# Kernel optimization log

Hardware: AMD Instinct MI355X
Metric: run time of the kernel (lower is better)

Reference implementation:

```python
import jax, jax.numpy as jnp
import numpy as np

WSCALE = 0.02  # keep conv outputs / softmax logits in a sane range

def _conv3x3(x, w):
    # x: [B,C,H,W], w: [O,I,3,3], stride 1, padding 1 (SAME), no bias
    return jax.lax.conv_general_dilated(
        x, w, window_strides=(1, 1), padding='SAME',
        dimension_numbers=('NCHW', 'OIHW', 'NCHW'))

def setup_inputs() -> dict:
    key = jax.random.key(0)
    ks = jax.random.split(key, 5)
    B, C, V, T = 8, 256, 256, 64
    Cq, C1 = C // 8, C // 2
    x = jax.random.normal(ks[0], (B, C, V, T), dtype=jnp.float32)
    wq = jax.random.normal(ks[1], (Cq, C, 3, 3), dtype=jnp.float32) * WSCALE
    wk = jax.random.normal(ks[2], (Cq, C, 3, 3), dtype=jnp.float32) * WSCALE
    wv = jax.random.normal(ks[3], (C1, C, 3, 3), dtype=jnp.float32) * WSCALE
    wo = jax.random.normal(ks[4], (C, C1, 3, 3), dtype=jnp.float32) * WSCALE
    sigma = jnp.ones((1,), dtype=jnp.float32)
    return {'x': x, 'wq': wq, 'wk': wk, 'wv': wv, 'wo': wo, 'sigma': sigma}

def reference(x, wq, wk, wv, wo, sigma):
    # x: [B, C, V, T]; attention over V, independent per (B, T) slice
    q = _conv3x3(x, wq)   # [B, Cq, V, T]
    k = _conv3x3(x, wk)   # [B, Cq, V, T]
    v = _conv3x3(x, wv)   # [B, C1, V, T]
    # permute(0,3,2,1): [B, T, V, C]
    q = jnp.transpose(q, (0, 3, 2, 1))
    k = jnp.transpose(k, (0, 3, 2, 1))
    v = jnp.transpose(v, (0, 3, 2, 1))
    # scores: [B, T, V, V]; softmax over last dim (original softmax dim=2 of [B*T,V,V])
    attn = jax.nn.softmax(jnp.einsum('btvc,btuc->btvu', q, k), axis=-1)
    av = jnp.einsum('btvu,btuc->btvc', attn, v)        # [B, T, V, C1]
    av = jnp.transpose(av, (0, 3, 2, 1))               # [B, C1, V, T]
    out = _conv3x3(av, wo)                             # [B, C, V, T]
    return x + sigma * out
```

## Files before the change

kernel.cpp:

```cpp
#include <hip/hip_runtime.h>
#include <hip/hip_bf16.h>
#include <cstdint>

#define B_  8
#define C_  256
#define V_  256
#define T_  64
#define CQ_ 32
#define C1_ 128

typedef float  floatx4 __attribute__((ext_vector_type(4)));
typedef __bf16 bf16x8  __attribute__((ext_vector_type(8)));

static __device__ __forceinline__ ushort f2bf(float f) {
    union { float f; uint32_t u; } cv; cv.f = f;
    const uint32_t u = cv.u;
    return (ushort)((u + 0x7FFFu + ((u >> 16) & 1u)) >> 16);
}
static __device__ __forceinline__ void bf2x(uint32_t p, float& f0, float& f1) {
    union { uint32_t u; float f; } a, b;
    a.u = p << 16; b.u = p & 0xffff0000u;
    f0 = a.f; f1 = b.f;
}

__global__ __launch_bounds__(256) void transpose_x(
    const float* __restrict__ x, ushort* __restrict__ xT)
{
    __shared__ float xs[256 * 65];
    const int tid = threadIdx.x;
    const int v = blockIdx.x & 255;
    const int b = blockIdx.x >> 8;

    for (int i = tid; i < 16384; i += 256) {
        const int t = i & 63, c = i >> 6;
        xs[c * 65 + t] = x[(((size_t)b * C_ + c) * V_ + v) * T_ + t];
    }
    __syncthreads();
    for (int i = tid; i < 16384; i += 256) {
        const int c = i & 255, t = i >> 8;
        xT[(((size_t)b * V_ + v) * T_ + t) * C_ + c] = f2bf(xs[c * 65 + t]);
    }
}

__global__ __launch_bounds__(256) void pack_weights(
    const float* __restrict__ wq, const float* __restrict__ wk,
    const float* __restrict__ wv, const float* __restrict__ wo,
    ushort* __restrict__ Wqkv, ushort* __restrict__ Wo)
{
    const int r = blockIdx.x;
    const int tid = threadIdx.x;
    const float* src; ushort* dst; int Klen;
    if (r < 192) {
        if (r < 32)      src = wq + (size_t)r * 2304;
        else if (r < 64) src = wk + (size_t)(r - 32) * 2304;
        else             src = wv + (size_t)(r - 64) * 2304;
        dst = Wqkv + (size_t)r * 2304; Klen = 2304;
    } else {
        src = wo + (size_t)(r - 192) * 1152;
        dst = Wo + (size_t)(r - 192) * 1152; Klen = 1152;
    }
    for (int k = tid; k < Klen; k += 256) {
        const int cc = k / 288, rem = k % 288;
        const int tap = rem >> 5, ci = rem & 31;
        const int c = cc * 32 + ci;
        dst[k] = f2bf(src[c * 9 + tap]);
    }
}

__global__ __launch_bounds__(256) void conv_qkv_mfma(
    const ushort* __restrict__ xT, const ushort* __restrict__ Wqkv,
    ushort* __restrict__ qb, ushort* __restrict__ kb, ushort* __restrict__ vb)
{
    __shared__ __align__(16) ushort Bs[4 * 66 * 40];
    __shared__ __align__(16) ushort As[64 * 296];

    const int tid  = threadIdx.x;
    const int lane = tid & 63;
    const int wave = tid >> 6;
    const int wave_m = (wave >> 1) * 32;
    const int wave_n = (wave & 1) * 64;
    const int nl = lane & 15;
    const int q8 = lane >> 4;

    int idx = blockIdx.x;
    const int og = idx % 3; idx /= 3;
    const int v2 = idx & 127;
    const int b  = idx >> 7;
    const int v0 = v2 * 2;

    floatx4 acc[2][4];
    #pragma unroll
    for (int i = 0; i < 2; i++)
        #pragma unroll
        for (int j = 0; j < 4; j++) acc[i][j] = (floatx4)0.f;

    const int rr = tid >> 6, ts = tid & 63;
    const int vsrc = v0 - 1 + rr;
    const int ar = tid >> 2, sub = tid & 3;

    for (int cc = 0; cc < 8; cc++) {
        const int c0 = cc * 32;
        __syncthreads();
        {
            ushort* bdst = &Bs[(rr * 66 + 1 + ts) * 40];
            if (vsrc >= 0 && vsrc < V_) {
                const ushort* src = &xT[(((size_t)b * V_ + vsrc) * T_ + ts) * C_ + c0];
                *(uint4*)(bdst + 0)  = *(const uint4*)(src + 0);
                *(uint4*)(bdst + 8)  = *(const uint4*)(src + 8);
                *(uint4*)(bdst + 16) = *(const uint4*)(src + 16);
                *(uint4*)(bdst + 24) = *(const uint4*)(src + 24);
            } else {
                const uint4 z = {0u, 0u, 0u, 0u};
                *(uint4*)(bdst + 0) = z; *(uint4*)(bdst + 8) = z;
                *(uint4*)(bdst + 16) = z; *(uint4*)(bdst + 24) = z;
            }
            if (tid < 8) {
                const int r2 = tid >> 1, side = (tid & 1) * 65;
                ushort* zp = &Bs[(r2 * 66 + side) * 40];
                const uint4 z = {0u, 0u, 0u, 0u};
                *(uint4*)(zp + 0) = z; *(uint4*)(zp + 8) = z;
                *(uint4*)(zp + 16) = z; *(uint4*)(zp + 24) = z;
            }
        }
        {
            const ushort* asrc = &Wqkv[(size_t)(og * 64 + ar) * 2304 + cc * 288];
            ushort* adst = &As[ar * 296];
            #pragma unroll
            for (int j = 0; j < 9; j++) {
                const int w8 = (sub + j * 4) * 8;
                *(uint4*)(adst + w8) = *(const uint4*)(asrc + w8);
            }
        }
        __syncthreads();

        #pragma unroll
        for (int tap = 0; tap < 9; tap++) {
            const int dv = tap / 3, dt = tap % 3;
            const bf16x8 a0 = *(const bf16x8*)&As[(wave_m + nl) * 296 + tap * 32 + q8 * 8];
            const bf16x8 a1 = *(const bf16x8*)&As[(wave_m + 16 + nl) * 296 + tap * 32 + q8 * 8];
            #pragma unroll
            for (int nt = 0; nt < 4; nt++) {
                const int n0 = wave_n + nt * 16;
                const int vv = n0 >> 6, tt0 = n0 & 63;
                const bf16x8 bf = *(const bf16x8*)
                    &Bs[((vv + dv) * 66 + tt0 + nl + dt) * 40 + q8 * 8];
                acc[0][nt] = __builtin_amdgcn_mfma_f32_16x16x32_bf16(a0, bf, acc[0][nt], 0, 0, 0);
                acc[1][nt] = __builtin_amdgcn_mfma_f32_16x16x32_bf16(a1, bf, acc[1][nt], 0, 0, 0);
            }
        }
    }

    #pragma unroll
    for (int mt = 0; mt < 2; mt++) {
        const int g0 = og * 64 + wave_m + mt * 16 + q8 * 4;
        ushort* buf; int cbase, Cb;
        if (g0 < 32)      { buf = qb; cbase = g0;      Cb = CQ_; }
        else if (g0 < 64) { buf = kb; cbase = g0 - 32; Cb = CQ_; }
        else              { buf = vb; cbase = g0 - 64; Cb = C1_; }
        #pragma unroll
        for (int nt = 0; nt < 4; nt++) {
            const int n = wave_n + nt * 16 + nl;
            const int vv = n >> 6, tt = n & 63;
            const floatx4 A = acc[mt][nt];
            ushort4 o;
            o.x = f2bf(A[0]); o.y = f2bf(A[1]); o.z = f2bf(A[2]); o.w = f2bf(A[3]);
            *(ushort4*)&buf[(((size_t)b * V_ + v0 + vv) * T_ + tt) * Cb + cbase] = o;
        }
    }
}

__global__ __launch_bounds__(256) void conv_o_mfma(
    const ushort* __restrict__ avT, const ushort* __restrict__ Wo,
    const float* __restrict__ x, const float* __restrict__ sigma,
    float* __restrict__ out)
{
    __shared__ __align__(16) ushort Bs[4 * 66 * 40];
    __shared__ __align__(16) ushort As[64 * 296];

    const int tid  = threadIdx.x;
    const int lane = tid & 63;
    const int wave = tid >> 6;
    const int wave_m = (wave >> 1) * 32;
    const int wave_n = (wave & 1) * 64;
    const int nl = lane & 15;
    const int q8 = lane >> 4;

    int idx = blockIdx.x;
    const int og = idx & 3; idx >>= 2;
    const int v2 = idx & 127;
    const int b  = idx >> 7;
    const int v0 = v2 * 2;

    floatx4 acc[2][4];
    #pragma unroll
    for (int i = 0; i < 2; i++)
        #pragma unroll
        for (int j = 0; j < 4; j++) acc[i][j] = (floatx4)0.f;

    const int rr = tid >> 6, ts = tid & 63;
    const int vsrc = v0 - 1 + rr;
    const int ar = tid >> 2, sub = tid & 3;

    for (int cc = 0; cc < 4; cc++) {
        const int c0 = cc * 32;
        __syncthreads();
        {
            ushort* bdst = &Bs[(rr * 66 + 1 + ts) * 40];
            if (vsrc >= 0 && vsrc < V_) {
                const ushort* src = &avT[(((size_t)b * V_ + vsrc) * T_ + ts) * C1_ + c0];
                *(uint4*)(bdst + 0)  = *(const uint4*)(src + 0);
                *(uint4*)(bdst + 8)  = *(const uint4*)(src + 8);
                *(uint4*)(bdst + 16) = *(const uint4*)(src + 16);
                *(uint4*)(bdst + 24) = *(const uint4*)(src + 24);
            } else {
                const uint4 z = {0u, 0u, 0u, 0u};
                *(uint4*)(bdst + 0) = z; *(uint4*)(bdst + 8) = z;
                *(uint4*)(bdst + 16) = z; *(uint4*)(bdst + 24) = z;
            }
            if (tid < 8) {
                const int r2 = tid >> 1, side = (tid & 1) * 65;
                ushort* zp = &Bs[(r2 * 66 + side) * 40];
                const uint4 z = {0u, 0u, 0u, 0u};
                *(uint4*)(zp + 0) = z; *(uint4*)(zp + 8) = z;
                *(uint4*)(zp + 16) = z; *(uint4*)(zp + 24) = z;
            }
        }
        {
            const ushort* asrc = &Wo[(size_t)(og * 64 + ar) * 1152 + cc * 288];
            ushort* adst = &As[ar * 296];
            #pragma unroll
            for (int j = 0; j < 9; j++) {
                const int w8 = (sub + j * 4) * 8;
                *(uint4*)(adst + w8) = *(const uint4*)(asrc + w8);
            }
        }
        __syncthreads();

        #pragma unroll
        for (int tap = 0; tap < 9; tap++) {
            const int dv = tap / 3, dt = tap % 3;
            const bf16x8 a0 = *(const bf16x8*)&As[(wave_m + nl) * 296 + tap * 32 + q8 * 8];
            const bf16x8 a1 = *(const bf16x8*)&As[(wave_m + 16 + nl) * 296 + tap * 32 + q8 * 8];
            #pragma unroll
            for (int nt = 0; nt < 4; nt++) {
                const int n0 = wave_n + nt * 16;
                const int vv = n0 >> 6, tt0 = n0 & 63;
                const bf16x8 bf = *(const bf16x8*)
                    &Bs[((vv + dv) * 66 + tt0 + nl + dt) * 40 + q8 * 8];
                acc[0][nt] = __builtin_amdgcn_mfma_f32_16x16x32_bf16(a0, bf, acc[0][nt], 0, 0, 0);
                acc[1][nt] = __builtin_amdgcn_mfma_f32_16x16x32_bf16(a1, bf, acc[1][nt], 0, 0, 0);
            }
        }
    }

    const float sg = sigma[0];
    #pragma unroll
    for (int mt = 0; mt < 2; mt++) {
        const int cb = og * 64 + wave_m + mt * 16 + q8 * 4;
        #pragma unroll
        for (int nt = 0; nt < 4; nt++) {
            const int n = wave_n + nt * 16 + nl;
            const int vv = n >> 6, tt = n & 63;
            const floatx4 A = acc[mt][nt];
            #pragma unroll
            for (int r = 0; r < 4; r++) {
                const size_t o = (((size_t)b * C_ + cb + r) * V_ + (v0 + vv)) * T_ + tt;
                out[o] = x[o] + sg * A[r];
            }
        }
    }
}

#define L2E 1.44269504f

__global__ __launch_bounds__(256, 1) void attn_mfma(
    const ushort* __restrict__ qb, const ushort* __restrict__ kb,
    const ushort* __restrict__ vb, ushort* __restrict__ avT)
{
    __shared__ __align__(16) ushort Ksh[256 * 40];
    __shared__ __align__(16) ushort Vt[128 * 264];
    __shared__ __align__(16) ushort Psh[4][64 * 72];

    const int tid  = threadIdx.x;
    const int lane = tid & 63;
    const int w    = tid >> 6;
    const int l15  = lane & 15;
    const int q8   = lane >> 4;
    const int bt = blockIdx.x;
    const int b = bt >> 6, t = bt & 63;

    {
        const ushort* kp = &kb[(((size_t)b * 256 + tid) * 64 + t) * 32];
        #pragma unroll
        for (int j = 0; j < 4; j++)
            *(uint4*)&Ksh[tid * 40 + j * 8] = *(const uint4*)(kp + j * 8);
    }
    {
        const int c8 = tid & 15;
        #pragma unroll
        for (int it = 0; it < 8; it++) {
            const int up = it * 16 + (tid >> 4);
            const ushort* vp0 = &vb[(((size_t)b * 256 + up * 2) * 64 + t) * 128 + c8 * 8];
            uint4 ra = *(const uint4*)vp0;
            uint4 rb = *(const uint4*)(vp0 + 64 * 128);
            const ushort* pa = (const ushort*)&ra;
            const ushort* pb = (const ushort*)&rb;
            const int g = up >> 2, sub = up & 3;
            #pragma unroll
            for (int j = 0; j < 8; j++) {
                const int c = c8 * 8 + j;
                const uint word = (uint)pa[j] | ((uint)pb[j] << 16);
                *(uint*)((char*)(Vt + c * 264) + ((g ^ (c8 & 7)) * 16 + sub * 4)) = word;
            }
        }
    }
    bf16x8 qf[4];
    #pragma unroll
    for (int vt = 0; vt < 4; vt++) {
        const int v = w * 64 + vt * 16 + l15;
        qf[vt] = *(const bf16x8*)&qb[(((size_t)b * 256 + v) * 64 + t) * 32 + q8 * 8];
    }
    __syncthreads();

    floatx4 accO[8][4];
    #pragma unroll
    for (int ct = 0; ct < 8; ct++)
        #pragma unroll
        for (int vt = 0; vt < 4; vt++) accO[ct][vt] = (floatx4)0.f;
    float m2[4] = {-3e38f, -3e38f, -3e38f, -3e38f};
    float lr[4] = {0.f, 0.f, 0.f, 0.f};
    ushort* Pw = Psh[w];

    for (int ch = 0; ch < 4; ch++) {
        const int u0 = ch * 64;
        floatx4 s[4][4];
        #pragma unroll
        for (int ut = 0; ut < 4; ut++) {
            const bf16x8 kf = *(const bf16x8*)&Ksh[(u0 + ut * 16 + l15) * 40 + q8 * 8];
            #pragma unroll
            for (int vt = 0; vt < 4; vt++) {
                floatx4 z = (floatx4)0.f;
                s[ut][vt] = __builtin_amdgcn_mfma_f32_16x16x32_bf16(kf, qf[vt], z, 0, 0, 0);
            }
        }
        #pragma unroll
        for (int vt = 0; vt < 4; vt++) {
            #pragma unroll
            for (int ut = 0; ut < 4; ut++)
                #pragma unroll
                for (int r = 0; r < 4; r++) s[ut][vt][r] *= L2E;
            float cm = -3e38f;
            #pragma unroll
            for (int ut = 0; ut < 4; ut++)
                #pragma unroll
                for (int r = 0; r < 4; r++) cm = fmaxf(cm, s[ut][vt][r]);
            cm = fmaxf(cm, __shfl_xor(cm, 16));
            cm = fmaxf(cm, __shfl_xor(cm, 32));
            const float mn = fmaxf(m2[vt], cm);
            const float alpha = __builtin_amdgcn_exp2f(m2[vt] - mn);
            float csum = 0.f;
            #pragma unroll
            for (int ut = 0; ut < 4; ut++)
                #pragma unroll
                for (int r = 0; r < 4; r++) {
                    const float p = __builtin_amdgcn_exp2f(s[ut][vt][r] - mn);
                    s[ut][vt][r] = p;
                    csum += p;
                }
            csum += __shfl_xor(csum, 16);
            csum += __shfl_xor(csum, 32);
            lr[vt] = lr[vt] * alpha + csum;
            m2[vt] = mn;
            #pragma unroll
            for (int ct = 0; ct < 8; ct++)
                #pragma unroll
                for (int r = 0; r < 4; r++) accO[ct][vt][r] *= alpha;
            const int vrow = vt * 16 + l15;
            #pragma unroll
            for (int ut = 0; ut < 4; ut++) {
                const uint w01 = (uint)f2bf(s[ut][vt][0]) | ((uint)f2bf(s[ut][vt][1]) << 16);
                const uint w23 = (uint)f2bf(s[ut][vt][2]) | ((uint)f2bf(s[ut][vt][3]) << 16);
                ushort* pp = Pw + vrow * 72 + ut * 16 + q8 * 4;
                *(uint*)pp = w01;
                *(uint*)(pp + 2) = w23;
            }
        }
        #pragma unroll
        for (int kc = 0; kc < 2; kc++) {
            bf16x8 pf[4];
            #pragma unroll
            for (int vt = 0; vt < 4; vt++)
                pf[vt] = *(const bf16x8*)&Pw[(vt * 16 + l15) * 72 + kc * 32 + q8 * 8];
            #pragma unroll
            for (int ct = 0; ct < 8; ct++) {
                const int c = ct * 16 + l15;
                const int ublk = (u0 + kc * 32) / 8 + q8;
                const bf16x8 vf = *(const bf16x8*)
                    ((const char*)(Vt + c * 264) + ((ublk ^ ((c >> 3) & 7)) * 16));
                #pragma unroll
                for (int vt = 0; vt < 4; vt++)
                    accO[ct][vt] = __builtin_amdgcn_mfma_f32_16x16x32_bf16(vf, pf[vt], accO[ct][vt], 0, 0, 0);
            }
        }
    }

    float inv[4];
    #pragma unroll
    for (int vt = 0; vt < 4; vt++) inv[vt] = 1.f / lr[vt];

    #pragma unroll
    for (int half = 0; half < 2; half++) {
        #pragma unroll
        for (int ct4 = 0; ct4 < 4; ct4++) {
            const int ct = half * 4 + ct4;
            #pragma unroll
            for (int vt = 0; vt < 4; vt++) {
                ushort4 o;
                o.x = f2bf(accO[ct][vt][0] * inv[vt]);
                o.y = f2bf(accO[ct][vt][1] * inv[vt]);
                o.z = f2bf(accO[ct][vt][2] * inv[vt]);
                o.w = f2bf(accO[ct][vt][3] * inv[vt]);
                *(ushort4*)&Pw[(vt * 16 + l15) * 72 + ct4 * 16 + q8 * 4] = o;
            }
        }
        const size_t dst = (((size_t)b * 256 + w * 64 + lane) * 64 + t) * 128 + half * 64;
        #pragma unroll
        for (int j = 0; j < 8; j++)
            *(uint4*)&avT[dst + j * 8] = *(const uint4*)&Pw[lane * 72 + j * 8];
    }
}

extern "C" void kernel_launch(void* const* d_in, const int* in_sizes, int n_in,
                              void* d_out, int out_size, void* d_ws, size_t ws_size,
                              hipStream_t stream)
{
    const float* x     = (const float*)d_in[0];
    const float* wq    = (const float*)d_in[1];
    const float* wk    = (const float*)d_in[2];
    const float* wv    = (const float*)d_in[3];
    const float* wo    = (const float*)d_in[4];
    const float* sigma = (const float*)d_in[5];
    float* out = (float*)d_out;

    ushort* ws   = (ushort*)d_ws;
    ushort* xT   = ws;  ws += (size_t)B_ * V_ * T_ * C_;
    ushort* qb   = ws;  ws += (size_t)B_ * V_ * T_ * CQ_;
    ushort* kb   = ws;  ws += (size_t)B_ * V_ * T_ * CQ_;
    ushort* vb   = ws;  ws += (size_t)B_ * V_ * T_ * C1_;
    ushort* avT  = ws;  ws += (size_t)B_ * V_ * T_ * C1_;
    ushort* Wqkv = ws;  ws += 192 * 2304;
    ushort* Wo   = ws;  ws += 256 * 1152;

    transpose_x <<<B_ * V_, 256, 0, stream>>>(x, xT);
    pack_weights<<<448, 256, 0, stream>>>(wq, wk, wv, wo, Wqkv, Wo);
    conv_qkv_mfma<<<B_ * 128 * 3, 256, 0, stream>>>(xT, Wqkv, qb, kb, vb);
    attn_mfma   <<<B_ * T_, 256, 0, stream>>>(qb, kb, vb, avT);
    conv_o_mfma <<<B_ * 128 * 4, 256, 0, stream>>>(avT, Wo, x, sigma, out);
}
```

Before: 580.3 us.

## Prepack weights in MFMA fragment order and restructure conv tiles with register prefetch

Weights are repacked into per-lane MFMA A-fragment order so the conv kernels read A operands straight from global/L2 instead of staging them in shared memory. Each block now covers 4 V rows (one per wave) and all 64 output channels, using a 6-row halo in LDS. The next channel chunk's activations are prefetched into registers while the current chunk computes. This removes the LDS traffic and barriers for weights and cuts halo redundancy, at the cost of more accumulator registers and more global weight reads per wave.

New measurement: 504.6 us. 1.15x faster.

```diff
diff --git a/kernel.cpp b/kernel.cpp
--- a/kernel.cpp
+++ b/kernel.cpp
@@ -17,11 +17,6 @@
     const uint32_t u = cv.u;
     return (ushort)((u + 0x7FFFu + ((u >> 16) & 1u)) >> 16);
 }
-static __device__ __forceinline__ void bf2x(uint32_t p, float& f0, float& f1) {
-    union { uint32_t u; float f; } a, b;
-    a.u = p << 16; b.u = p & 0xffff0000u;
-    f0 = a.f; f1 = b.f;
-}
 
 __global__ __launch_bounds__(256) void transpose_x(
     const float* __restrict__ x, ushort* __restrict__ xT)
@@ -47,23 +42,36 @@
     const float* __restrict__ wv, const float* __restrict__ wo,
     ushort* __restrict__ Wqkv, ushort* __restrict__ Wo)
 {
-    const int r = blockIdx.x;
-    const int tid = threadIdx.x;
-    const float* src; ushort* dst; int Klen;
-    if (r < 192) {
-        if (r < 32)      src = wq + (size_t)r * 2304;
-        else if (r < 64) src = wk + (size_t)(r - 32) * 2304;
-        else             src = wv + (size_t)(r - 64) * 2304;
-        dst = Wqkv + (size_t)r * 2304; Klen = 2304;
-    } else {
-        src = wo + (size_t)(r - 192) * 1152;
-        dst = Wo + (size_t)(r - 192) * 1152; Klen = 1152;
-    }
-    for (int k = tid; k < Klen; k += 256) {
-        const int cc = k / 288, rem = k % 288;
-        const int tap = rem >> 5, ci = rem & 31;
-        const int c = cc * 32 + ci;
-        dst[k] = f2bf(src[c * 9 + tap]);
+    const int tid = blockIdx.x * 256 + threadIdx.x;
+    const int total1 = 442368, total2 = 294912;
+    for (int idx = tid; idx < total1 + total2; idx += gridDim.x * 256) {
+        if (idx < total1) {
+            int i = idx;
+            const int e = i & 7;      i >>= 3;
+            const int lane = i & 63;  i >>= 6;
+            const int mtile = i & 3;  i >>= 2;
+            const int tap = i % 9;    i /= 9;
+            const int cc = i & 7;
+            const int og = i >> 3;
+            const int r = og * 64 + mtile * 16 + (lane & 15);
+            const int c = cc * 32 + (lane >> 4) * 8 + e;
+            const float* srow;
+            if (r < 32)      srow = wq + (size_t)r * 2304;
+            else if (r < 64) srow = wk + (size_t)(r - 32) * 2304;
+            else             srow = wv + (size_t)(r - 64) * 2304;
+            Wqkv[idx] = f2bf(srow[c * 9 + tap]);
+        } else {
+            int i = idx - total1;
+            const int e = i & 7;      i >>= 3;
+            const int lane = i & 63;  i >>= 6;
+            const int mtile = i & 3;  i >>= 2;
+            const int tap = i % 9;    i /= 9;
+            const int cc = i & 3;
+            const int og = i >> 2;
+            const int r = og * 64 + mtile * 16 + (lane & 15);
+            const int c = cc * 32 + (lane >> 4) * 8 + e;
+            Wo[idx - total1] = f2bf(wo[(size_t)r * 1152 + c * 9 + tap]);
+        }
     }
 }
 
@@ -71,100 +79,103 @@
     const ushort* __restrict__ xT, const ushort* __restrict__ Wqkv,
     ushort* __restrict__ qb, ushort* __restrict__ kb, ushort* __restrict__ vb)
 {
-    __shared__ __align__(16) ushort Bs[4 * 66 * 40];
-    __shared__ __align__(16) ushort As[64 * 296];
+    __shared__ __align__(16) ushort Bs[6 * 66 * 40];
 
     const int tid  = threadIdx.x;
     const int lane = tid & 63;
-    const int wave = tid >> 6;
-    const int wave_m = (wave >> 1) * 32;
-    const int wave_n = (wave & 1) * 64;
-    const int nl = lane & 15;
-    const int q8 = lane >> 4;
-
-    int idx = blockIdx.x;
-    const int og = idx % 3; idx /= 3;
-    const int v2 = idx & 127;
-    const int b  = idx >> 7;
-    const int v0 = v2 * 2;
-
-    floatx4 acc[2][4];
-    #pragma unroll
-    for (int i = 0; i < 2; i++)
+    const int w    = tid >> 6;
+    const int nl   = lane & 15;
+    const int q8   = lane >> 4;
+
+    const int og  = blockIdx.x >> 9;
+    const int rem = blockIdx.x & 511;
+    const int vg  = rem >> 3;
+    const int b   = rem & 7;
+    const int v0  = vg * 4;
+
+    floatx4 acc[4][4];
+    #pragma unroll
+    for (int i = 0; i < 4; i++)
         #pragma unroll
         for (int j = 0; j < 4; j++) acc[i][j] = (floatx4)0.f;
 
-    const int rr = tid >> 6, ts = tid & 63;
-    const int vsrc = v0 - 1 + rr;
-    const int ar = tid >> 2, sub = tid & 3;
+    const int t4 = tid >> 2, c4 = tid & 3;
+    ushort* const bdst = &Bs[(1 + t4) * 40 + c4 * 8];
+    const ushort* const xb  = &xT[(((size_t)b * V_) * T_ + t4) * C_ + c4 * 8];
+    const ushort* const Wog = Wqkv + (size_t)og * 147456 + lane * 8;
+
+    if (tid < 12) {
+        const int r = tid >> 1, side = (tid & 1) * 65;
+        ushort* zp = &Bs[(r * 66 + side) * 40];
+        const uint4 z = {0u, 0u, 0u, 0u};
+        *(uint4*)(zp + 0) = z; *(uint4*)(zp + 8) = z;
+        *(uint4*)(zp + 16) = z; *(uint4*)(zp + 24) = z;
+    }
+
+    const uint4 z4 = {0u, 0u, 0u, 0u};
+    uint4 s0, s1, s2, s3, s4, s5;
+
+#define QPF(CC) do {                                                          \
+    const int co_ = (CC) * 32;                                                \
+    s0 = (v0 >= 1)  ? *(const uint4*)(xb + (size_t)(v0 - 1) * (T_ * C_) + co_) : z4; \
+    s1 =              *(const uint4*)(xb + (size_t)(v0    ) * (T_ * C_) + co_);      \
+    s2 =              *(const uint4*)(xb + (size_t)(v0 + 1) * (T_ * C_) + co_);      \
+    s3 =              *(const uint4*)(xb + (size_t)(v0 + 2) * (T_ * C_) + co_);      \
+    s4 =              *(const uint4*)(xb + (size_t)(v0 + 3) * (T_ * C_) + co_);      \
+    s5 = (v0 < 252) ? *(const uint4*)(xb + (size_t)(v0 + 4) * (T_ * C_) + co_) : z4; \
+} while (0)
+
+    QPF(0);
 
     for (int cc = 0; cc < 8; cc++) {
-        const int c0 = cc * 32;
         __syncthreads();
-        {
-            ushort* bdst = &Bs[(rr * 66 + 1 + ts) * 40];
-            if (vsrc >= 0 && vsrc < V_) {
-                const ushort* src = &xT[(((size_t)b * V_ + vsrc) * T_ + ts) * C_ + c0];
-                *(uint4*)(bdst + 0)  = *(const uint4*)(src + 0);
-                *(uint4*)(bdst + 8)  = *(const uint4*)(src + 8);
-                *(uint4*)(bdst + 16) = *(const uint4*)(src + 16);
-                *(uint4*)(bdst + 24) = *(const uint4*)(src + 24);
-            } else {
-                const uint4 z = {0u, 0u, 0u, 0u};
-                *(uint4*)(bdst + 0) = z; *(uint4*)(bdst + 8) = z;
-                *(uint4*)(bdst + 16) = z; *(uint4*)(bdst + 24) = z;
-            }
-            if (tid < 8) {
-                const int r2 = tid >> 1, side = (tid & 1) * 65;
-                ushort* zp = &Bs[(r2 * 66 + side) * 40];
-                const uint4 z = {0u, 0u, 0u, 0u};
-                *(uint4*)(zp + 0) = z; *(uint4*)(zp + 8) = z;
-                *(uint4*)(zp + 16) = z; *(uint4*)(zp + 24) = z;
-            }
-        }
-        {
-            const ushort* asrc = &Wqkv[(size_t)(og * 64 + ar) * 2304 + cc * 288];
-            ushort* adst = &As[ar * 296];
-            #pragma unroll
-            for (int j = 0; j < 9; j++) {
-                const int w8 = (sub + j * 4) * 8;
-                *(uint4*)(adst + w8) = *(const uint4*)(asrc + w8);
-            }
-        }
+        *(uint4*)(bdst + 0 * 2640) = s0;
+        *(uint4*)(bdst + 1 * 2640) = s1;
+        *(uint4*)(bdst + 2 * 2640) = s2;
+        *(uint4*)(bdst + 3 * 2640) = s3;
+        *(uint4*)(bdst + 4 * 2640) = s4;
+        *(uint4*)(bdst + 5 * 2640) = s5;
         __syncthreads();
-
+        if (cc < 7) QPF(cc + 1);
+
+        const ushort* const Wcc = Wog + cc * 18432;
         #pragma unroll
         for (int tap = 0; tap < 9; tap++) {
             const int dv = tap / 3, dt = tap % 3;
-            const bf16x8 a0 = *(const bf16x8*)&As[(wave_m + nl) * 296 + tap * 32 + q8 * 8];
-            const bf16x8 a1 = *(const bf16x8*)&As[(wave_m + 16 + nl) * 296 + tap * 32 + q8 * 8];
+            bf16x8 bfr[4];
+            #pragma unroll
+            for (int nt = 0; nt < 4; nt++)
+                bfr[nt] = *(const bf16x8*)
+                    &Bs[((w + dv) * 66 + nt * 16 + nl + dt) * 40 + q8 * 8];
+            const bf16x8 a0 = *(const bf16x8*)(Wcc + tap * 2048 + 0 * 512);
+            const bf16x8 a1 = *(const bf16x8*)(Wcc + tap * 2048 + 1 * 512);
+            const bf16x8 a2 = *(const bf16x8*)(Wcc + tap * 2048 + 2 * 512);
+            const bf16x8 a3 = *(const bf16x8*)(Wcc + tap * 2048 + 3 * 512);
             #pragma unroll
             for (int nt = 0; nt < 4; nt++) {
-                const int n0 = wave_n + nt * 16;
-                const int vv = n0 >> 6, tt0 = n0 & 63;
-                const bf16x8 bf = *(const bf16x8*)
-                    &Bs[((vv + dv) * 66 + tt0 + nl + dt) * 40 + q8 * 8];
-                acc[0][nt] = __builtin_amdgcn_mfma_f32_16x16x32_bf16(a0, bf, acc[0][nt], 0, 0, 0);
-                acc[1][nt] = __builtin_amdgcn_mfma_f32_16x16x32_bf16(a1, bf, acc[1][nt], 0, 0, 0);
-            }
-        }
-    }
-
-    #pragma unroll
-    for (int mt = 0; mt < 2; mt++) {
-        const int g0 = og * 64 + wave_m + mt * 16 + q8 * 4;
+                acc[0][nt] = __builtin_amdgcn_mfma_f32_16x16x32_bf16(a0, bfr[nt], acc[0][nt], 0, 0, 0);
+                acc[1][nt] = __builtin_amdgcn_mfma_f32_16x16x32_bf16(a1, bfr[nt], acc[1][nt], 0, 0, 0);
+                acc[2][nt] = __builtin_amdgcn_mfma_f32_16x16x32_bf16(a2, bfr[nt], acc[2][nt], 0, 0, 0);
+                acc[3][nt] = __builtin_amdgcn_mfma_f32_16x16x32_bf16(a3, bfr[nt], acc[3][nt], 0, 0, 0);
+            }
+        }
+    }
+#undef QPF
+
+    #pragma unroll
+    for (int mt = 0; mt < 4; mt++) {
+        const int g0 = og * 64 + mt * 16 + q8 * 4;
         ushort* buf; int cbase, Cb;
         if (g0 < 32)      { buf = qb; cbase = g0;      Cb = CQ_; }
         else if (g0 < 64) { buf = kb; cbase = g0 - 32; Cb = CQ_; }
         else              { buf = vb; cbase = g0 - 64; Cb = C1_; }
         #pragma unroll
         for (int nt = 0; nt < 4; nt++) {
-            const int n = wave_n + nt * 16 + nl;
-            const int vv = n >> 6, tt = n & 63;
+            const int tt = nt * 16 + nl;
             const floatx4 A = acc[mt][nt];
             ushort4 o;
             o.x = f2bf(A[0]); o.y = f2bf(A[1]); o.z = f2bf(A[2]); o.w = f2bf(A[3]);
-            *(ushort4*)&buf[(((size_t)b * V_ + v0 + vv) * T_ + tt) * Cb + cbase] = o;
+            *(ushort4*)&buf[(((size_t)b * V_ + v0 + w) * T_ + tt) * Cb + cbase] = o;
         }
     }
 }
@@ -174,97 +185,100 @@
     const float* __restrict__ x, const float* __restrict__ sigma,
     float* __restrict__ out)
 {
-    __shared__ __align__(16) ushort Bs[4 * 66 * 40];
-    __shared__ __align__(16) ushort As[64 * 296];
+    __shared__ __align__(16) ushort Bs[6 * 66 * 40];
 
     const int tid  = threadIdx.x;
     const int lane = tid & 63;
-    const int wave = tid >> 6;
-    const int wave_m = (wave >> 1) * 32;
-    const int wave_n = (wave & 1) * 64;
-    const int nl = lane & 15;
-    const int q8 = lane >> 4;
-
-    int idx = blockIdx.x;
-    const int og = idx & 3; idx >>= 2;
-    const int v2 = idx & 127;
-    const int b  = idx >> 7;
-    const int v0 = v2 * 2;
-
-    floatx4 acc[2][4];
-    #pragma unroll
-    for (int i = 0; i < 2; i++)
+    const int w    = tid >> 6;
+    const int nl   = lane & 15;
+    const int q8   = lane >> 4;
+
+    const int og  = blockIdx.x >> 9;
+    const int rem = blockIdx.x & 511;
+    const int vg  = rem >> 3;
+    const int b   = rem & 7;
+    const int v0  = vg * 4;
+
+    floatx4 acc[4][4];
+    #pragma unroll
+    for (int i = 0; i < 4; i++)
         #pragma unroll
         for (int j = 0; j < 4; j++) acc[i][j] = (floatx4)0.f;
 
-    const int rr = tid >> 6, ts = tid & 63;
-    const int vsrc = v0 - 1 + rr;
-    const int ar = tid >> 2, sub = tid & 3;
+    const int t4 = tid >> 2, c4 = tid & 3;
+    ushort* const bdst = &Bs[(1 + t4) * 40 + c4 * 8];
+    const ushort* const ab  = &avT[(((size_t)b * V_) * T_ + t4) * C1_ + c4 * 8];
+    const ushort* const Wog = Wo + (size_t)og * 73728 + lane * 8;
+
+    if (tid < 12) {
+        const int r = tid >> 1, side = (tid & 1) * 65;
+        ushort* zp = &Bs[(r * 66 + side) * 40];
+        const uint4 z = {0u, 0u, 0u, 0u};
+        *(uint4*)(zp + 0) = z; *(uint4*)(zp + 8) = z;
+        *(uint4*)(zp + 16) = z; *(uint4*)(zp + 24) = z;
+    }
+
+    const uint4 z4 = {0u, 0u, 0u, 0u};
+    uint4 s0, s1, s2, s3, s4, s5;
+
+#define OPF(CC) do {                                                          \
+    const int co_ = (CC) * 32;                                                \
+    s0 = (v0 >= 1)  ? *(const uint4*)(ab + (size_t)(v0 - 1) * (T_ * C1_) + co_) : z4; \
+    s1 =              *(const uint4*)(ab + (size_t)(v0    ) * (T_ * C1_) + co_);      \
+    s2 =              *(const uint4*)(ab + (size_t)(v0 + 1) * (T_ * C1_) + co_);      \
+    s3 =              *(const uint4*)(ab + (size_t)(v0 + 2) * (T_ * C1_) + co_);      \
+    s4 =              *(const uint4*)(ab + (size_t)(v0 + 3) * (T_ * C1_) + co_);      \
+    s5 = (v0 < 252) ? *(const uint4*)(ab + (size_t)(v0 + 4) * (T_ * C1_) + co_) : z4; \
+} while (0)
+
+    OPF(0);
 
     for (int cc = 0; cc < 4; cc++) {
-        const int c0 = cc * 32;
         __syncthreads();
-        {
-            ushort* bdst = &Bs[(rr * 66 + 1 + ts) * 40];
-            if (vsrc >= 0 && vsrc < V_) {
-                const ushort* src = &avT[(((size_t)b * V_ + vsrc) * T_ + ts) * C1_ + c0];
-                *(uint4*)(bdst + 0)  = *(const uint4*)(src + 0);
-                *(uint4*)(bdst + 8)  = *(const uint4*)(src + 8);
-                *(uint4*)(bdst + 16) = *(const uint4*)(src + 16);
-                *(uint4*)(bdst + 24) = *(const uint4*)(src + 24);
-            } else {
-                const uint4 z = {0u, 0u, 0u, 0u};
-                *(uint4*)(bdst + 0) = z; *(uint4*)(bdst + 8) = z;
-                *(uint4*)(bdst + 16) = z; *(uint4*)(bdst + 24) = z;
-            }
-            if (tid < 8) {
-                const int r2 = tid >> 1, side = (tid & 1) * 65;
-                ushort* zp = &Bs[(r2 * 66 + side) * 40];
-                const uint4 z = {0u, 0u, 0u, 0u};
-                *(uint4*)(zp + 0) = z; *(uint4*)(zp + 8) = z;
-                *(uint4*)(zp + 16) = z; *(uint4*)(zp + 24) = z;
-            }
-        }
-        {
-            const ushort* asrc = &Wo[(size_t)(og * 64 + ar) * 1152 + cc * 288];
-            ushort* adst = &As[ar * 296];
-            #pragma unroll
-            for (int j = 0; j < 9; j++) {
-                const int w8 = (sub + j * 4) * 8;
-                *(uint4*)(adst + w8) = *(const uint4*)(asrc + w8);
-            }
-        }
+        *(uint4*)(bdst + 0 * 2640) = s0;
+        *(uint4*)(bdst + 1 * 2640) = s1;
+        *(uint4*)(bdst + 2 * 2640) = s2;
+        *(uint4*)(bdst + 3 * 2640) = s3;
+        *(uint4*)(bdst + 4 * 2640) = s4;
+        *(uint4*)(bdst + 5 * 2640) = s5;
         __syncthreads();
-
+        if (cc < 3) OPF(cc + 1);
+
+        const ushort* const Wcc = Wog + cc * 18432;
         #pragma unroll
         for (int tap = 0; tap < 9; tap++) {
             const int dv = tap / 3, dt = tap % 3;
-            const bf16x8 a0 = *(const bf16x8*)&As[(wave_m + nl) * 296 + tap * 32 + q8 * 8];
-            const bf16x8 a1 = *(const bf16x8*)&As[(wave_m + 16 + nl) * 296 + tap * 32 + q8 * 8];
+            bf16x8 bfr[4];
+            #pragma unroll
+            for (int nt = 0; nt < 4; nt++)
+                bfr[nt] = *(const bf16x8*)
+                    &Bs[((w + dv) * 66 + nt * 16 + nl + dt) * 40 + q8 * 8];
+            const bf16x8 a0 = *(const bf16x8*)(Wcc + tap * 2048 + 0 * 512);
+            const bf16x8 a1 = *(const bf16x8*)(Wcc + tap * 2048 + 1 * 512);
+            const bf16x8 a2 = *(const bf16x8*)(Wcc + tap * 2048 + 2 * 512);
+            const bf16x8 a3 = *(const bf16x8*)(Wcc + tap * 2048 + 3 * 512);
             #pragma unroll
             for (int nt = 0; nt < 4; nt++) {
-                const int n0 = wave_n + nt * 16;
-                const int vv = n0 >> 6, tt0 = n0 & 63;
-                const bf16x8 bf = *(const bf16x8*)
-                    &Bs[((vv + dv) * 66 + tt0 + nl + dt) * 40 + q8 * 8];
-                acc[0][nt] = __builtin_amdgcn_mfma_f32_16x16x32_bf16(a0, bf, acc[0][nt], 0, 0, 0);
-                acc[1][nt] = __builtin_amdgcn_mfma_f32_16x16x32_bf16(a1, bf, acc[1][nt], 0, 0, 0);
-            }
-        }
-    }
+                acc[0][nt] = __builtin_amdgcn_mfma_f32_16x16x32_bf16(a0, bfr[nt], acc[0][nt], 0, 0, 0);
+                acc[1][nt] = __builtin_amdgcn_mfma_f32_16x16x32_bf16(a1, bfr[nt], acc[1][nt], 0, 0, 0);
+                acc[2][nt] = __builtin_amdgcn_mfma_f32_16x16x32_bf16(a2, bfr[nt], acc[2][nt], 0, 0, 0);
+                acc[3][nt] = __builtin_amdgcn_mfma_f32_16x16x32_bf16(a3, bfr[nt], acc[3][nt], 0, 0, 0);
+            }
+        }
+    }
+#undef OPF
 
     const float sg = sigma[0];
     #pragma unroll
-    for (int mt = 0; mt < 2; mt++) {
-        const int cb = og * 64 + wave_m + mt * 16 + q8 * 4;
+    for (int mt = 0; mt < 4; mt++) {
+        const int cb = og * 64 + mt * 16 + q8 * 4;
         #pragma unroll
         for (int nt = 0; nt < 4; nt++) {
-            const int n = wave_n + nt * 16 + nl;
-            const int vv = n >> 6, tt = n & 63;
+            const int tt = nt * 16 + nl;
             const floatx4 A = acc[mt][nt];
             #pragma unroll
             for (int r = 0; r < 4; r++) {
-                const size_t o = (((size_t)b * C_ + cb + r) * V_ + (v0 + vv)) * T_ + tt;
+                const size_t o = (((size_t)b * C_ + cb + r) * V_ + (v0 + w)) * T_ + tt;
                 out[o] = x[o] + sg * A[r];
             }
         }
@@ -448,12 +462,12 @@
     ushort* kb   = ws;  ws += (size_t)B_ * V_ * T_ * CQ_;
     ushort* vb   = ws;  ws += (size_t)B_ * V_ * T_ * C1_;
     ushort* avT  = ws;  ws += (size_t)B_ * V_ * T_ * C1_;
-    ushort* Wqkv = ws;  ws += 192 * 2304;
-    ushort* Wo   = ws;  ws += 256 * 1152;
+    ushort* Wqkv = ws;  ws += 442368;
+    ushort* Wo   = ws;  ws += 294912;
 
     transpose_x <<<B_ * V_, 256, 0, stream>>>(x, xT);
     pack_weights<<<448, 256, 0, stream>>>(wq, wk, wv, wo, Wqkv, Wo);
-    conv_qkv_mfma<<<B_ * 128 * 3, 256, 0, stream>>>(xT, Wqkv, qb, kb, vb);
+    conv_qkv_mfma<<<3 * 512, 256, 0, stream>>>(xT, Wqkv, qb, kb, vb);
     attn_mfma   <<<B_ * T_, 256, 0, stream>>>(qb, kb, vb, avT);
-    conv_o_mfma <<<B_ * 128 * 4, 256, 0, stream>>>(avT, Wo, x, sigma, out);
-}
+    conv_o_mfma <<<4 * 512, 256, 0, stream>>>(avT, Wo, x, sigma, out);
+}
```
